# Kernel optimization log

Measured on AMD Instinct MI355X. Metric: run time of the kernel, lower is better.

## Reference

```python
import jax, jax.numpy as jnp
import numpy as np

N = 50000          # nodes
E = 800000         # edges (before self-loops)
G = 64             # graphs in the batch
IN, HID, HEADS, OUT = 512, 128, 2, 64
NEG_SLOPE = 0.2
BN_EPS = 1e-5


def gat_conv(x, src, dst, W, a_src, a_dst, b, concat):
    """PyG-style GATConv (shared lin for src/dst, leaky-relu scoring,
    segment-softmax over incoming edges per destination node)."""
    n = x.shape[0]
    H, C = a_src.shape
    xl = (x @ W).reshape(n, H, C)                      # [N,H,C]
    es = (xl * a_src).sum(-1)                          # [N,H] alpha_src
    ed = (xl * a_dst).sum(-1)                          # [N,H] alpha_dst
    e = jax.nn.leaky_relu(es[src] + ed[dst], NEG_SLOPE)  # [E,H]
    m = jax.ops.segment_max(e, dst, num_segments=n)    # stable softmax
    ex = jnp.exp(e - m[dst])
    den = jax.ops.segment_sum(ex, dst, num_segments=n)
    alpha = ex / (den[dst] + 1e-16)                    # [E,H]
    out = jax.ops.segment_sum(xl[src] * alpha[:, :, None], dst, num_segments=n)
    out = out.reshape(n, H * C) if concat else out.mean(axis=1)
    return out + b


def batch_norm(x, g, b):
    mu = x.mean(axis=0)
    var = x.var(axis=0)  # biased, as torch BN uses for normalization
    return (x - mu) * jax.lax.rsqrt(var + BN_EPS) * g + b


def setup_inputs() -> dict:
    key = jax.random.key(0)
    ks = jax.random.split(key, 24)
    HC = HID * HEADS
    inp = {
        'x': jax.random.normal(ks[0], (N, IN), jnp.float32),
        'edge_index': jax.random.randint(ks[1], (2, E), 0, N, jnp.int64) if jax.config.jax_enable_x64 else jax.random.randint(ks[1], (2, E), 0, N).astype(jnp.int32),
        'batch': jnp.sort(jax.random.randint(ks[2], (N,), 0, G)).astype(jnp.int32),
        # conv1: 512 -> (2,128) concat -> 256
        'W1': jax.random.normal(ks[3], (IN, HC), jnp.float32) * (1.0 / np.sqrt(IN)),
        'as1': jax.random.normal(ks[4], (HEADS, HID), jnp.float32) * 0.05,
        'ad1': jax.random.normal(ks[5], (HEADS, HID), jnp.float32) * 0.05,
        'b1': jnp.zeros((HC,), jnp.float32),
        'g1': jnp.ones((HC,), jnp.float32),
        'be1': jnp.zeros((HC,), jnp.float32),
        # conv2: 256 -> (2,128) concat -> 256
        'W2': jax.random.normal(ks[6], (HC, HC), jnp.float32) * (1.0 / np.sqrt(HC)),
        'as2': jax.random.normal(ks[7], (HEADS, HID), jnp.float32) * 0.05,
        'ad2': jax.random.normal(ks[8], (HEADS, HID), jnp.float32) * 0.05,
        'b2': jnp.zeros((HC,), jnp.float32),
        'g2': jnp.ones((HC,), jnp.float32),
        'be2': jnp.zeros((HC,), jnp.float32),
        # conv3: 256 -> (1,128) mean -> 128
        'W3': jax.random.normal(ks[9], (HC, HID), jnp.float32) * (1.0 / np.sqrt(HC)),
        'as3': jax.random.normal(ks[10], (1, HID), jnp.float32) * 0.05,
        'ad3': jax.random.normal(ks[11], (1, HID), jnp.float32) * 0.05,
        'b3': jnp.zeros((HID,), jnp.float32),
        # final linear 128 -> 64
        'Wlin': jax.random.normal(ks[12], (HID, OUT), jnp.float32) * (1.0 / np.sqrt(HID)),
        'blin': jnp.zeros((OUT,), jnp.float32),
    }
    return inp


def reference(x, edge_index, batch, W1, as1, ad1, b1, g1, be1,
              W2, as2, ad2, b2, g2, be2, W3, as3, ad3, b3, Wlin, blin):
    # add self-loops (PyG GATConv default)
    loop = jnp.arange(N, dtype=edge_index.dtype)
    src = jnp.concatenate([edge_index[0], loop])
    dst = jnp.concatenate([edge_index[1], loop])

    h = gat_conv(x, src, dst, W1, as1, ad1, b1, concat=True)
    h = jax.nn.relu(batch_norm(h, g1, be1))           # dropout: eval mode (identity)
    h = gat_conv(h, src, dst, W2, as2, ad2, b2, concat=True)
    h = jax.nn.relu(batch_norm(h, g2, be2))
    h = gat_conv(h, src, dst, W3, as3, ad3, b3, concat=False)  # [N,128]

    # global mean pool over graphs
    cnt = jax.ops.segment_sum(jnp.ones((N,), h.dtype), batch, num_segments=G)
    pooled = jax.ops.segment_sum(h, batch, num_segments=G) / jnp.maximum(cnt, 1.0)[:, None]
    return pooled @ Wlin + blin                        # [G,64]
```

## Files before the change

### kernel.cpp

```cpp
#include <hip/hip_runtime.h>
#include <cstdint>
#include <math.h>

#define NN 50000
#define EE 800000
#define GG 64
#define NEG_SLOPE 0.2f
#define BN_EPS 1e-5f

typedef short bf16x8 __attribute__((ext_vector_type(8)));
typedef float f32x4 __attribute__((ext_vector_type(4)));

__global__ void k_memset32(int* p, int val, int n) {
    int i = blockIdx.x * blockDim.x + threadIdx.x;
    int stride = gridDim.x * blockDim.x;
    for (; i < n; i += stride) p[i] = val;
}

__device__ inline float leaky(float x) { return x > 0.f ? x : NEG_SLOPE * x; }

__device__ inline unsigned short f2bf(float f) {
    union { float f; uint32_t u; } v;
    v.f = f;
    uint32_t u = v.u;
    return (unsigned short)((u + 0x7fffu + ((u >> 16) & 1u)) >> 16);
}

__device__ inline float bf2f(unsigned short u) {
    union { uint32_t u; float f; } v;
    v.u = (uint32_t)u << 16;
    return v.f;
}
__device__ inline float bflo(uint32_t u) { return __uint_as_float(u << 16); }
__device__ inline float bfhi(uint32_t u) { return __uint_as_float(u & 0xffff0000u); }
__device__ inline uint32_t packbf(float a, float b) {
    return (uint32_t)f2bf(a) | ((uint32_t)f2bf(b) << 16);
}

__device__ inline unsigned char f2fp8(float v) {
    int p = __builtin_amdgcn_cvt_pk_fp8_f32(v, v, 0, false);
    return (unsigned char)(p & 0xff);
}

__device__ inline void gload16(const void* g, void* l) {
    __builtin_amdgcn_global_load_lds(
        (const __attribute__((address_space(1))) unsigned int*)g,
        (__attribute__((address_space(3))) unsigned int*)l, 16, 0, 0);
}

__global__ void k_convert_bf16(const float* __restrict__ in, unsigned short* __restrict__ out,
                               int n4) {
    int i = blockIdx.x * blockDim.x + threadIdx.x;
    int stride = gridDim.x * blockDim.x;
    for (; i < n4; i += stride) {
        float4 v = ((const float4*)in)[i];
        uint2 o;
        o.x = packbf(v.x, v.y);
        o.y = packbf(v.z, v.w);
        ((uint2*)out)[i] = o;
    }
}

__global__ void k_transpose_all(const float* __restrict__ W1, const float* __restrict__ W2,
                                const float* __restrict__ W3, unsigned short* __restrict__ Wt1,
                                unsigned short* __restrict__ Wt2, unsigned short* __restrict__ Wt3) {
    int idx = blockIdx.x * 256 + threadIdx.x;
    if (idx < 512 * 256) {
        int k = idx >> 8, m_ = idx & 255;
        Wt1[(size_t)m_ * 512 + k] = f2bf(W1[idx]);
    } else if (idx < 512 * 256 + 256 * 256) {
        int i = idx - 512 * 256;
        int k = i >> 8, m_ = i & 255;
        Wt2[(size_t)m_ * 256 + k] = f2bf(W2[i]);
    } else if (idx < 512 * 256 + 256 * 256 + 256 * 128) {
        int i = idx - (512 * 256 + 256 * 256);
        int k = i >> 7, m_ = i & 127;
        Wt3[(size_t)m_ * 256 + k] = f2bf(W3[i]);
    }
}

__global__ __launch_bounds__(256) void k_gemm_mfma(
        const unsigned short* __restrict__ A, const unsigned short* __restrict__ Bt,
        unsigned char* __restrict__ C8,
        const float* __restrict__ asrc, const float* __restrict__ adst,
        float* __restrict__ es, float* __restrict__ ed,
        int NR, int K, int M, int H, int gxc) {
    __shared__ unsigned short As[2][128 * 32];
    __shared__ unsigned short Bs[2][128 * 32];
    __shared__ float esA[2][128], edA[2][128];
    int tid = threadIdx.x;
    int wave = tid >> 6, lane = tid & 63;
    int r16 = lane & 15, kg = lane >> 4;
    int wr = wave >> 1, wc = wave & 1;

    int nwg = gridDim.x;
    int nb = blockIdx.x;
    int q = nwg >> 3, r = nwg & 7;
    int xcd = nb & 7, ii = nb >> 3;
    int w = (xcd < r ? xcd * (q + 1) : r * (q + 1) + (xcd - r) * q) + ii;
    int rowBase = (w / gxc) * 128;
    int colBase = (w % gxc) * 128;

    const unsigned short* gA[2];
    const unsigned short* gB[2];
#pragma unroll
    for (int it = 0; it < 2; ++it) {
        int j = it * 256 + tid;
        int row = j >> 2, slot = j & 3;
        int ss = slot ^ ((row >> 1) & 3);
        int rg = rowBase + row;
        if (rg >= NR) rg = NR - 1;
        gA[it] = A + (size_t)rg * K + ss * 8;
        gB[it] = Bt + (size_t)(colBase + row) * K + ss * 8;
    }

    auto STAGE = [&](int buf, int k0) {
#pragma unroll
        for (int it = 0; it < 2; ++it) {
            unsigned short* lbase = &As[buf][(it * 256 + wave * 64) * 8];
            gload16(gA[it] + k0, lbase);
            unsigned short* lbase2 = &Bs[buf][(it * 256 + wave * 64) * 8];
            gload16(gB[it] + k0, lbase2);
        }
    };

    f32x4 acc[4][4] = {};
    int nt = K >> 5;
    STAGE(0, 0);
    __syncthreads();
    for (int t = 0; t < nt; ++t) {
        int cur = t & 1;
        if (t + 1 < nt) STAGE(cur ^ 1, (t + 1) << 5);
        bf16x8 af[4], bfr[4];
#pragma unroll
        for (int m = 0; m < 4; m++) {
            int row = wr * 64 + m * 16 + r16;
            af[m] = *(const bf16x8*)&As[cur][row * 32 + (kg ^ ((row >> 1) & 3)) * 8];
        }
#pragma unroll
        for (int n = 0; n < 4; n++) {
            int row = wc * 64 + n * 16 + r16;
            bfr[n] = *(const bf16x8*)&Bs[cur][row * 32 + (kg ^ ((row >> 1) & 3)) * 8];
        }
#pragma unroll
        for (int m = 0; m < 4; m++)
#pragma unroll
            for (int n = 0; n < 4; n++)
                acc[m][n] = __builtin_amdgcn_mfma_f32_16x16x32_bf16(af[m], bfr[n], acc[m][n], 0, 0, 0);
        __syncthreads();
    }
    int crow0 = rowBase + wr * 64;
    int ccol = colBase + wc * 64 + r16;
#pragma unroll
    for (int m = 0; m < 4; m++) {
#pragma unroll
        for (int j = 0; j < 4; j++) {
            int row = crow0 + m * 16 + kg * 4 + j;
            if (row < NR) {
#pragma unroll
                for (int n = 0; n < 4; n++)
                    C8[(size_t)row * M + ccol + n * 16] = f2fp8(acc[m][n][j]);
            }
        }
    }
    int h_blk = colBase >> 7;
    float as_[4], ad_[4];
#pragma unroll
    for (int n = 0; n < 4; n++) {
        int ch = wc * 64 + n * 16 + r16;
        as_[n] = asrc[h_blk * 128 + ch];
        ad_[n] = adst[h_blk * 128 + ch];
    }
#pragma unroll
    for (int m = 0; m < 4; m++) {
#pragma unroll
        for (int j = 0; j < 4; j++) {
            float e1 = 0.f, e2 = 0.f;
#pragma unroll
            for (int n = 0; n < 4; n++) {
                e1 += acc[m][n][j] * as_[n];
                e2 += acc[m][n][j] * ad_[n];
            }
#pragma unroll
            for (int mask = 1; mask < 16; mask <<= 1) {
                e1 += __shfl_xor(e1, mask, 64);
                e2 += __shfl_xor(e2, mask, 64);
            }
            if (r16 == 0) {
                int lr = wr * 64 + m * 16 + kg * 4 + j;
                esA[wc][lr] = e1;
                edA[wc][lr] = e2;
            }
        }
    }
    __syncthreads();
    if (tid < 128) {
        int row = rowBase + tid;
        if (row < NR) {
            es[row * H + h_blk] = esA[0][tid] + esA[1][tid];
            ed[row * H + h_blk] = edA[0][tid] + edA[1][tid];
        }
    }
}

template <int VEC>
__device__ inline void edge_load(const unsigned char* rp, uint2& w) {
    if constexpr (VEC == 8) {
        w = *(const uint2*)rp;
    } else {
        w.x = *(const unsigned int*)rp;
        w.y = 0;
    }
}

template <int VEC>
__device__ inline void edge_acc(float* acc, float e, const uint2& w) {
    auto p0 = __builtin_amdgcn_cvt_pk_f32_fp8(w.x, false);
    auto p1 = __builtin_amdgcn_cvt_pk_f32_fp8(w.x, true);
    acc[0] += e * p0[0]; acc[1] += e * p0[1];
    acc[2] += e * p1[0]; acc[3] += e * p1[1];
    if constexpr (VEC == 8) {
        auto p2 = __builtin_amdgcn_cvt_pk_f32_fp8(w.y, false);
        auto p3 = __builtin_amdgcn_cvt_pk_f32_fp8(w.y, true);
        acc[4] += e * p2[0]; acc[5] += e * p2[1];
        acc[6] += e * p3[0]; acc[7] += e * p3[1];
    }
}

template <int VEC, int H>
__global__ __launch_bounds__(256) void k_aggregate(
        const unsigned char* __restrict__ xl, const float* __restrict__ es,
        const float* __restrict__ ed, const int* __restrict__ offsets,
        const int* __restrict__ count, const int* __restrict__ ssrc,
        const float* __restrict__ bias, unsigned short* __restrict__ out) {
    const int M = 32 * VEC;
    int wid = threadIdx.x >> 6;
    int n = blockIdx.x * 4 + wid;
    if (n >= NN) return;
    int lane = threadIdx.x & 63;
    int half = lane >> 5, l32 = lane & 31;
    int c0 = l32 * VEC;
    int h = (H == 2) ? (c0 >> 7) : 0;

    float edn0, edn1 = 0.f, self0, self1 = 0.f;
    if constexpr (H == 2) {
        float2 edp = *(const float2*)&ed[n * 2];
        float2 esp = *(const float2*)&es[n * 2];
        edn0 = edp.x; edn1 = edp.y;
        self0 = __expf(leaky(esp.x + edn0));
        self1 = __expf(leaky(esp.y + edn1));
    } else {
        edn0 = ed[n];
        self0 = __expf(leaky(es[n] + edn0));
    }
    float ex_self = (H == 2 && h == 1) ? self1 : self0;

    float acc[VEC] = {};
    if (half == 0) {
        uint2 w;
        edge_load<VEC>(xl + (size_t)n * M + c0, w);
        edge_acc<VEC>(acc, ex_self, w);
    }

    __shared__ int ls[4][64];
    __shared__ float le[4][H][64];
    float den0 = 0.f, den1 = 0.f;
    int s0 = offsets[n], cnt = count[n];
    for (int base = 0; base < cnt; base += 64) {
        int i = base + lane;
        int s = 0;
        float e0 = 0.f, e1 = 0.f;
        if (i < cnt) {
            s = ssrc[s0 + i];
            if constexpr (H == 2) {
                float2 esp = *(const float2*)&es[s * 2];
                e0 = __expf(leaky(esp.x + edn0)); den0 += e0;
                e1 = __expf(leaky(esp.y + edn1)); den1 += e1;
            } else {
                e0 = __expf(leaky(es[s] + edn0)); den0 += e0;
            }
        }
        ls[wid][lane] = s;
        le[wid][0][lane] = e0;
        if constexpr (H == 2) le[wid][1][lane] = e1;
        asm volatile("s_waitcnt lgkmcnt(0)" ::: "memory");
        int lim = min(64, cnt - base);
        int j = half;
        for (; j + 7 < lim; j += 8) {
            int sA = ls[wid][j], sB = ls[wid][j + 2], sC = ls[wid][j + 4], sD = ls[wid][j + 6];
            float eA = le[wid][h][j], eB = le[wid][h][j + 2];
            float eC = le[wid][h][j + 4], eD = le[wid][h][j + 6];
            uint2 wA, wB, wC, wD;
            edge_load<VEC>(xl + (size_t)sA * M + c0, wA);
            edge_load<VEC>(xl + (size_t)sB * M + c0, wB);
            edge_load<VEC>(xl + (size_t)sC * M + c0, wC);
            edge_load<VEC>(xl + (size_t)sD * M + c0, wD);
            edge_acc<VEC>(acc, eA, wA);
            edge_acc<VEC>(acc, eB, wB);
            edge_acc<VEC>(acc, eC, wC);
            edge_acc<VEC>(acc, eD, wD);
        }
        for (; j < lim; j += 2) {
            int sA = ls[wid][j];
            float eA = le[wid][h][j];
            uint2 wA;
            edge_load<VEC>(xl + (size_t)sA * M + c0, wA);
            edge_acc<VEC>(acc, eA, wA);
        }
    }

#pragma unroll
    for (int off = 32; off > 0; off >>= 1) {
        den0 += __shfl_xor(den0, off, 64);
        if constexpr (H == 2) den1 += __shfl_xor(den1, off, 64);
    }
#pragma unroll
    for (int v = 0; v < VEC; v++) acc[v] += __shfl_xor(acc[v], 32, 64);

    float den = ((H == 2 && h == 1) ? den1 : den0) + ex_self + 1e-16f;
    float inv = 1.f / den;
    if (half == 0) {
        unsigned short* op = out + (size_t)n * M + c0;
        if constexpr (VEC == 8) {
            uint4 o;
            o.x = packbf(acc[0] * inv + bias[c0 + 0], acc[1] * inv + bias[c0 + 1]);
            o.y = packbf(acc[2] * inv + bias[c0 + 2], acc[3] * inv + bias[c0 + 3]);
            o.z = packbf(acc[4] * inv + bias[c0 + 4], acc[5] * inv + bias[c0 + 5]);
            o.w = packbf(acc[6] * inv + bias[c0 + 6], acc[7] * inv + bias[c0 + 7]);
            *(uint4*)op = o;
        } else {
            uint2 o;
            o.x = packbf(acc[0] * inv + bias[c0 + 0], acc[1] * inv + bias[c0 + 1]);
            o.y = packbf(acc[2] * inv + bias[c0 + 2], acc[3] * inv + bias[c0 + 3]);
            *(uint2*)op = o;
        }
    }
}

__global__ void k_count(const int* __restrict__ dst, int* __restrict__ count) {
    int e = blockIdx.x * blockDim.x + threadIdx.x;
    if (e < EE) atomicAdd(&count[dst[e]], 1);
}

__global__ void k_scan_local(const int* __restrict__ in, int* __restrict__ out_excl,
                             int* __restrict__ bsums, int n) {
    __shared__ int s[256];
    int tid = threadIdx.x;
    int i = blockIdx.x * 256 + tid;
    int v = (i < n) ? in[i] : 0;
    s[tid] = v;
    __syncthreads();
    for (int off = 1; off < 256; off <<= 1) {
        int t_ = (tid >= off) ? s[tid - off] : 0;
        __syncthreads();
        s[tid] += t_;
        __syncthreads();
    }
    if (i < n) out_excl[i] = s[tid] - v;
    if (tid == 255) bsums[blockIdx.x] = s[255];
}

__global__ void k_scan_sums(int* __restrict__ b, int n) {
    __shared__ int s[256];
    int tid = threadIdx.x;
    int v = (tid < n) ? b[tid] : 0;
    s[tid] = v;
    __syncthreads();
    for (int off = 1; off < 256; off <<= 1) {
        int t_ = (tid >= off) ? s[tid - off] : 0;
        __syncthreads();
        s[tid] += t_;
        __syncthreads();
    }
    if (tid < n) b[tid] = s[tid] - v;
}

__global__ void k_scan_add(int* __restrict__ out_excl, const int* __restrict__ bsums, int n) {
    int i = blockIdx.x * 256 + threadIdx.x;
    if (i < n) out_excl[i] += bsums[blockIdx.x];
}

__global__ void k_scatter(const int* __restrict__ src, const int* __restrict__ dst,
                          const int* __restrict__ offsets, int* __restrict__ cursor,
                          int* __restrict__ ssrc) {
    int e = blockIdx.x * blockDim.x + threadIdx.x;
    if (e >= EE) return;
    int d = dst[e];
    int p = offsets[d] + atomicAdd(&cursor[d], 1);
    ssrc[p] = src[e];
}

__global__ __launch_bounds__(256) void k_bn_stats(const unsigned short* __restrict__ h,
                                                  float* __restrict__ part) {
    int tid = threadIdx.x;
    int bid = blockIdx.x;
    int c0 = (tid & 31) * 8;
    int rg = tid >> 5;
    float s[8] = {}, s2[8] = {};
    for (int r = bid * 8 + rg; r < NN; r += 2048) {
        uint4 v = *(const uint4*)(h + (size_t)r * 256 + c0);
        float f;
        f = bflo(v.x); s[0] += f; s2[0] += f * f;
        f = bfhi(v.x); s[1] += f; s2[1] += f * f;
        f = bflo(v.y); s[2] += f; s2[2] += f * f;
        f = bfhi(v.y); s[3] += f; s2[3] += f * f;
        f = bflo(v.z); s[4] += f; s2[4] += f * f;
        f = bfhi(v.z); s[5] += f; s2[5] += f * f;
        f = bflo(v.w); s[6] += f; s2[6] += f * f;
        f = bfhi(v.w); s[7] += f; s2[7] += f * f;
    }
    __shared__ float sb[8][256];
#pragma unroll
    for (int v = 0; v < 8; v++) sb[rg][c0 + v] = s[v];
    __syncthreads();
    float tot = 0.f;
#pragma unroll
    for (int g = 0; g < 8; g++) tot += sb[g][tid];
    part[bid * 512 + tid] = tot;
    __syncthreads();
#pragma unroll
    for (int v = 0; v < 8; v++) sb[rg][c0 + v] = s2[v];
    __syncthreads();
    tot = 0.f;
#pragma unroll
    for (int g = 0; g < 8; g++) tot += sb[g][tid];
    part[bid * 512 + 256 + tid] = tot;
}

__global__ void k_bn_finalize(const float* __restrict__ part, const float* __restrict__ g,
                              const float* __restrict__ be, float* __restrict__ scale,
                              float* __restrict__ shift) {
    int t = threadIdx.x;
    float s = 0.f, s2 = 0.f;
    for (int b = 0; b < 256; b++) {
        s += part[b * 512 + t];
        s2 += part[b * 512 + 256 + t];
    }
    float mu = s / (float)NN;
    float var = s2 / (float)NN - mu * mu;
    float sc = g[t] * rsqrtf(var + BN_EPS);
    scale[t] = sc;
    shift[t] = be[t] - mu * sc;
}

__global__ void k_bn_apply(unsigned short* __restrict__ h, const float* __restrict__ scale,
                           const float* __restrict__ shift) {
    int i = blockIdx.x * blockDim.x + threadIdx.x;
    int stride = gridDim.x * blockDim.x;
    int total = NN * 256 / 8;
    uint4* h4 = (uint4*)h;
    for (; i < total; i += stride) {
        uint4 v = h4[i];
        int t = (i * 8) & 255;
        float f0 = fmaxf(bflo(v.x) * scale[t + 0] + shift[t + 0], 0.f);
        float f1 = fmaxf(bfhi(v.x) * scale[t + 1] + shift[t + 1], 0.f);
        float f2 = fmaxf(bflo(v.y) * scale[t + 2] + shift[t + 2], 0.f);
        float f3 = fmaxf(bfhi(v.y) * scale[t + 3] + shift[t + 3], 0.f);
        float f4 = fmaxf(bflo(v.z) * scale[t + 4] + shift[t + 4], 0.f);
        float f5 = fmaxf(bfhi(v.z) * scale[t + 5] + shift[t + 5], 0.f);
        float f6 = fmaxf(bflo(v.w) * scale[t + 6] + shift[t + 6], 0.f);
        float f7 = fmaxf(bfhi(v.w) * scale[t + 7] + shift[t + 7], 0.f);
        v.x = packbf(f0, f1);
        v.y = packbf(f2, f3);
        v.z = packbf(f4, f5);
        v.w = packbf(f6, f7);
        h4[i] = v;
    }
}

#define POOL_ROWS 128
__global__ void k_pool(const unsigned short* __restrict__ h3, const int* __restrict__ batch,
                       float* __restrict__ pooled, int* __restrict__ cnt) {
    int t = threadIdx.x;
    int r0 = blockIdx.x * POOL_ROWS;
    if (r0 >= NN) return;
    int rend = min(r0 + POOL_ROWS, NN);
    float acc = 0.f;
    int c_acc = 0;
    int g_cur = batch[r0];
    for (int r = r0; r < rend; r++) {
        int g = batch[r];
        if (g != g_cur) {
            atomicAdd(&pooled[g_cur * 128 + t], acc);
            if (t == 0) atomicAdd(&cnt[g_cur], c_acc);
            acc = 0.f;
            c_acc = 0;
            g_cur = g;
        }
        acc += bf2f(h3[(size_t)r * 128 + t]);
        c_acc++;
    }
    atomicAdd(&pooled[g_cur * 128 + t], acc);
    if (t == 0) atomicAdd(&cnt[g_cur], c_acc);
}

__global__ void k_final(const float* __restrict__ pooled, const int* __restrict__ cnt,
                        const float* __restrict__ Wlin, const float* __restrict__ blin,
                        float* __restrict__ out) {
    int g = blockIdx.x;
    int o = threadIdx.x;
    float c = (float)max(cnt[g], 1);
    float acc = 0.f;
    for (int k = 0; k < 128; k++) acc += pooled[g * 128 + k] * Wlin[k * 64 + o];
    out[g * 64 + o] = acc / c + blin[o];
}

extern "C" void kernel_launch(void* const* d_in, const int* in_sizes, int n_in,
                              void* d_out, int out_size, void* d_ws, size_t ws_size,
                              hipStream_t stream) {
    const float* x = (const float*)d_in[0];
    const int* ei = (const int*)d_in[1];
    const int* batch = (const int*)d_in[2];
    const float* W1 = (const float*)d_in[3];
    const float* as1 = (const float*)d_in[4];
    const float* ad1 = (const float*)d_in[5];
    const float* b1 = (const float*)d_in[6];
    const float* g1 = (const float*)d_in[7];
    const float* be1 = (const float*)d_in[8];
    const float* W2 = (const float*)d_in[9];
    const float* as2 = (const float*)d_in[10];
    const float* ad2 = (const float*)d_in[11];
    const float* b2 = (const float*)d_in[12];
    const float* g2 = (const float*)d_in[13];
    const float* be2 = (const float*)d_in[14];
    const float* W3 = (const float*)d_in[15];
    const float* as3 = (const float*)d_in[16];
    const float* ad3 = (const float*)d_in[17];
    const float* b3 = (const float*)d_in[18];
    const float* Wlin = (const float*)d_in[19];
    const float* blin = (const float*)d_in[20];
    float* out = (float*)d_out;

    const int* src = ei;
    const int* dst = ei + EE;

    char* ws = (char*)d_ws;
    size_t off = 0;
    auto alloc = [&](size_t bytes) -> void* {
        void* p = (void*)(ws + off);
        off = (off + bytes + 255) & ~(size_t)255;
        return p;
    };
    unsigned short* xb = (unsigned short*)alloc((size_t)NN * 512 * 2);
    unsigned char* xl = (unsigned char*)alloc((size_t)NN * 256);
    unsigned short* hbuf = (unsigned short*)alloc((size_t)NN * 256 * 2);
    unsigned short* Wt1 = (unsigned short*)alloc((size_t)256 * 512 * 2);
    unsigned short* Wt2 = (unsigned short*)alloc((size_t)256 * 256 * 2);
    unsigned short* Wt3 = (unsigned short*)alloc((size_t)128 * 256 * 2);
    float* es = (float*)alloc((size_t)NN * 2 * 4);
    float* ed = (float*)alloc((size_t)NN * 2 * 4);
    int* count = (int*)alloc((size_t)NN * 4);
    int* offsets = (int*)alloc((size_t)NN * 4);
    int* cursor = (int*)alloc((size_t)NN * 4);
    int* ssrc = (int*)alloc((size_t)EE * 4);
    int* bsums = (int*)alloc(256 * 4);
    float* bnpart = (float*)alloc((size_t)256 * 512 * 4);
    float* bnscale = (float*)alloc(256 * 4);
    float* bnshift = (float*)alloc(256 * 4);
    float* pooled = (float*)alloc(64 * 128 * 4);
    int* cnt = (int*)alloc(64 * 4);

    const int EB = (EE + 255) / 256;
    const int NB = (NN + 255) / 256;
    const int AGB = (NN + 3) / 4;
    const int NRB = (NN + 127) / 128;

    k_convert_bf16<<<2048, 256, 0, stream>>>(x, xb, NN * 512 / 4);
    k_transpose_all<<<(512 * 256 + 256 * 256 + 256 * 128 + 255) / 256, 256, 0, stream>>>(
        W1, W2, W3, Wt1, Wt2, Wt3);

    k_memset32<<<64, 256, 0, stream>>>(count, 0, NN);
    k_count<<<EB, 256, 0, stream>>>(dst, count);
    k_scan_local<<<NB, 256, 0, stream>>>(count, offsets, bsums, NN);
    k_scan_sums<<<1, 256, 0, stream>>>(bsums, NB);
    k_scan_add<<<NB, 256, 0, stream>>>(offsets, bsums, NN);
    k_memset32<<<64, 256, 0, stream>>>(cursor, 0, NN);
    k_scatter<<<EB, 256, 0, stream>>>(src, dst, offsets, cursor, ssrc);

    auto bn_relu = [&](unsigned short* h, const float* g_, const float* be_) {
        k_bn_stats<<<256, 256, 0, stream>>>(h, bnpart);
        k_bn_finalize<<<1, 256, 0, stream>>>(bnpart, g_, be_, bnscale, bnshift);
        k_bn_apply<<<1024, 256, 0, stream>>>(h, bnscale, bnshift);
    };

    k_gemm_mfma<<<2 * NRB, 256, 0, stream>>>(xb, Wt1, xl, as1, ad1, es, ed, NN, 512, 256, 2, 2);
    k_aggregate<8, 2><<<AGB, 256, 0, stream>>>(xl, es, ed, offsets, count, ssrc, b1, hbuf);
    bn_relu(hbuf, g1, be1);

    k_gemm_mfma<<<2 * NRB, 256, 0, stream>>>(hbuf, Wt2, xl, as2, ad2, es, ed, NN, 256, 256, 2, 2);
    k_aggregate<8, 2><<<AGB, 256, 0, stream>>>(xl, es, ed, offsets, count, ssrc, b2, hbuf);
    bn_relu(hbuf, g2, be2);

    k_gemm_mfma<<<NRB, 256, 0, stream>>>(hbuf, Wt3, xl, as3, ad3, es, ed, NN, 256, 128, 1, 1);
    k_aggregate<4, 1><<<AGB, 256, 0, stream>>>(xl, es, ed, offsets, count, ssrc, b3, hbuf);

    k_memset32<<<33, 256, 0, stream>>>((int*)pooled, 0, 64 * 128 + 64);
    k_pool<<<(NN + POOL_ROWS - 1) / POOL_ROWS, 128, 0, stream>>>(hbuf, batch, pooled, cnt);
    k_final<<<GG, 64, 0, stream>>>(pooled, cnt, Wlin, blin, out);
}
```

Measured before the change: 430.7 us.

## Fuse mean-pool into final aggregation, merge prep kernels, single-block scan

```diff
diff --git a/kernel.cpp b/kernel.cpp
--- a/kernel.cpp
+++ b/kernel.cpp
@@ -48,34 +48,34 @@
         (__attribute__((address_space(3))) unsigned int*)l, 16, 0, 0);
 }
 
-__global__ void k_convert_bf16(const float* __restrict__ in, unsigned short* __restrict__ out,
-                               int n4) {
-    int i = blockIdx.x * blockDim.x + threadIdx.x;
+__global__ void k_prep(const float* __restrict__ x, unsigned short* __restrict__ xb,
+                       const float* __restrict__ W1, const float* __restrict__ W2,
+                       const float* __restrict__ W3, unsigned short* __restrict__ Wt1,
+                       unsigned short* __restrict__ Wt2, unsigned short* __restrict__ Wt3) {
+    int t0 = blockIdx.x * blockDim.x + threadIdx.x;
     int stride = gridDim.x * blockDim.x;
-    for (; i < n4; i += stride) {
-        float4 v = ((const float4*)in)[i];
+    const int n4 = NN * 512 / 4;
+    for (int i = t0; i < n4; i += stride) {
+        float4 v = ((const float4*)x)[i];
         uint2 o;
         o.x = packbf(v.x, v.y);
         o.y = packbf(v.z, v.w);
-        ((uint2*)out)[i] = o;
-    }
-}
-
-__global__ void k_transpose_all(const float* __restrict__ W1, const float* __restrict__ W2,
-                                const float* __restrict__ W3, unsigned short* __restrict__ Wt1,
-                                unsigned short* __restrict__ Wt2, unsigned short* __restrict__ Wt3) {
-    int idx = blockIdx.x * 256 + threadIdx.x;
-    if (idx < 512 * 256) {
-        int k = idx >> 8, m_ = idx & 255;
-        Wt1[(size_t)m_ * 512 + k] = f2bf(W1[idx]);
-    } else if (idx < 512 * 256 + 256 * 256) {
-        int i = idx - 512 * 256;
-        int k = i >> 8, m_ = i & 255;
-        Wt2[(size_t)m_ * 256 + k] = f2bf(W2[i]);
-    } else if (idx < 512 * 256 + 256 * 256 + 256 * 128) {
-        int i = idx - (512 * 256 + 256 * 256);
-        int k = i >> 7, m_ = i & 127;
-        Wt3[(size_t)m_ * 256 + k] = f2bf(W3[i]);
+        ((uint2*)xb)[i] = o;
+    }
+    const int TR = 512 * 256 + 256 * 256 + 256 * 128;
+    for (int idx = t0; idx < TR; idx += stride) {
+        if (idx < 512 * 256) {
+            int k = idx >> 8, m_ = idx & 255;
+            Wt1[(size_t)m_ * 512 + k] = f2bf(W1[idx]);
+        } else if (idx < 512 * 256 + 256 * 256) {
+            int i = idx - 512 * 256;
+            int k = i >> 8, m_ = i & 255;
+            Wt2[(size_t)m_ * 256 + k] = f2bf(W2[i]);
+        } else {
+            int i = idx - (512 * 256 + 256 * 256);
+            int k = i >> 7, m_ = i & 127;
+            Wt3[(size_t)m_ * 256 + k] = f2bf(W3[i]);
+        }
     }
 }
 
@@ -227,12 +227,13 @@
     }
 }
 
-template <int VEC, int H>
+template <int VEC, int H, bool POOL>
 __global__ __launch_bounds__(256) void k_aggregate(
         const unsigned char* __restrict__ xl, const float* __restrict__ es,
         const float* __restrict__ ed, const int* __restrict__ offsets,
         const int* __restrict__ count, const int* __restrict__ ssrc,
-        const float* __restrict__ bias, unsigned short* __restrict__ out) {
+        const float* __restrict__ bias, unsigned short* __restrict__ out,
+        const int* __restrict__ batch, float* __restrict__ pooled, int* __restrict__ cnt) {
     const int M = 32 * VEC;
     int wid = threadIdx.x >> 6;
     int n = blockIdx.x * 4 + wid;
@@ -265,12 +266,12 @@
     __shared__ int ls[4][64];
     __shared__ float le[4][H][64];
     float den0 = 0.f, den1 = 0.f;
-    int s0 = offsets[n], cnt = count[n];
-    for (int base = 0; base < cnt; base += 64) {
+    int s0 = offsets[n], cnte = count[n];
+    for (int base = 0; base < cnte; base += 64) {
         int i = base + lane;
         int s = 0;
         float e0 = 0.f, e1 = 0.f;
-        if (i < cnt) {
+        if (i < cnte) {
             s = ssrc[s0 + i];
             if constexpr (H == 2) {
                 float2 esp = *(const float2*)&es[s * 2];
@@ -284,7 +285,7 @@
         le[wid][0][lane] = e0;
         if constexpr (H == 2) le[wid][1][lane] = e1;
         asm volatile("s_waitcnt lgkmcnt(0)" ::: "memory");
-        int lim = min(64, cnt - base);
+        int lim = min(64, cnte - base);
         int j = half;
         for (; j + 7 < lim; j += 8) {
             int sA = ls[wid][j], sB = ls[wid][j + 2], sC = ls[wid][j + 4], sD = ls[wid][j + 6];
@@ -320,19 +321,27 @@
     float den = ((H == 2 && h == 1) ? den1 : den0) + ex_self + 1e-16f;
     float inv = 1.f / den;
     if (half == 0) {
-        unsigned short* op = out + (size_t)n * M + c0;
-        if constexpr (VEC == 8) {
-            uint4 o;
-            o.x = packbf(acc[0] * inv + bias[c0 + 0], acc[1] * inv + bias[c0 + 1]);
-            o.y = packbf(acc[2] * inv + bias[c0 + 2], acc[3] * inv + bias[c0 + 3]);
-            o.z = packbf(acc[4] * inv + bias[c0 + 4], acc[5] * inv + bias[c0 + 5]);
-            o.w = packbf(acc[6] * inv + bias[c0 + 6], acc[7] * inv + bias[c0 + 7]);
-            *(uint4*)op = o;
+        if constexpr (POOL) {
+            int g = batch[n];
+            if (lane == 0) atomicAdd(&cnt[g], 1);
+#pragma unroll
+            for (int v = 0; v < VEC; v++)
+                atomicAdd(&pooled[g * 128 + c0 + v], acc[v] * inv + bias[c0 + v]);
         } else {
-            uint2 o;
-            o.x = packbf(acc[0] * inv + bias[c0 + 0], acc[1] * inv + bias[c0 + 1]);
-            o.y = packbf(acc[2] * inv + bias[c0 + 2], acc[3] * inv + bias[c0 + 3]);
-            *(uint2*)op = o;
+            unsigned short* op = out + (size_t)n * M + c0;
+            if constexpr (VEC == 8) {
+                uint4 o;
+                o.x = packbf(acc[0] * inv + bias[c0 + 0], acc[1] * inv + bias[c0 + 1]);
+                o.y = packbf(acc[2] * inv + bias[c0 + 2], acc[3] * inv + bias[c0 + 3]);
+                o.z = packbf(acc[4] * inv + bias[c0 + 4], acc[5] * inv + bias[c0 + 5]);
+                o.w = packbf(acc[6] * inv + bias[c0 + 6], acc[7] * inv + bias[c0 + 7]);
+                *(uint4*)op = o;
+            } else {
+                uint2 o;
+                o.x = packbf(acc[0] * inv + bias[c0 + 0], acc[1] * inv + bias[c0 + 1]);
+                o.y = packbf(acc[2] * inv + bias[c0 + 2], acc[3] * inv + bias[c0 + 3]);
+                *(uint2*)op = o;
+            }
         }
     }
 }
@@ -342,42 +351,38 @@
     if (e < EE) atomicAdd(&count[dst[e]], 1);
 }
 
-__global__ void k_scan_local(const int* __restrict__ in, int* __restrict__ out_excl,
-                             int* __restrict__ bsums, int n) {
-    __shared__ int s[256];
+__global__ __launch_bounds__(1024) void k_scan(const int* __restrict__ in,
+                                               int* __restrict__ out, int n) {
+    __shared__ int wsum[16];
     int tid = threadIdx.x;
-    int i = blockIdx.x * 256 + tid;
-    int v = (i < n) ? in[i] : 0;
-    s[tid] = v;
-    __syncthreads();
-    for (int off = 1; off < 256; off <<= 1) {
-        int t_ = (tid >= off) ? s[tid - off] : 0;
+    int wid = tid >> 6, lane = tid & 63;
+    int carry = 0;
+    for (int base = 0; base < n; base += 1024) {
+        int i = base + tid;
+        int v = (i < n) ? in[i] : 0;
+        int x = v;
+#pragma unroll
+        for (int off = 1; off < 64; off <<= 1) {
+            int y = __shfl_up(x, off, 64);
+            if (lane >= off) x += y;
+        }
+        if (lane == 63) wsum[wid] = x;
         __syncthreads();
-        s[tid] += t_;
+        if (wid == 0) {
+            int t = (lane < 16) ? wsum[lane] : 0;
+#pragma unroll
+            for (int off = 1; off < 16; off <<= 1) {
+                int y = __shfl_up(t, off, 64);
+                if (lane >= off) t += y;
+            }
+            if (lane < 16) wsum[lane] = t;
+        }
         __syncthreads();
-    }
-    if (i < n) out_excl[i] = s[tid] - v;
-    if (tid == 255) bsums[blockIdx.x] = s[255];
-}
-
-__global__ void k_scan_sums(int* __restrict__ b, int n) {
-    __shared__ int s[256];
-    int tid = threadIdx.x;
-    int v = (tid < n) ? b[tid] : 0;
-    s[tid] = v;
-    __syncthreads();
-    for (int off = 1; off < 256; off <<= 1) {
-        int t_ = (tid >= off) ? s[tid - off] : 0;
+        int woff = (wid > 0) ? wsum[wid - 1] : 0;
+        if (i < n) out[i] = carry + woff + x - v;
+        carry += wsum[15];
         __syncthreads();
-        s[tid] += t_;
-        __syncthreads();
-    }
-    if (tid < n) b[tid] = s[tid] - v;
-}
-
-__global__ void k_scan_add(int* __restrict__ out_excl, const int* __restrict__ bsums, int n) {
-    int i = blockIdx.x * 256 + threadIdx.x;
-    if (i < n) out_excl[i] += bsums[blockIdx.x];
+    }
 }
 
 __global__ void k_scatter(const int* __restrict__ src, const int* __restrict__ dst,
@@ -466,32 +471,6 @@
         v.w = packbf(f6, f7);
         h4[i] = v;
     }
-}
-
-#define POOL_ROWS 128
-__global__ void k_pool(const unsigned short* __restrict__ h3, const int* __restrict__ batch,
-                       float* __restrict__ pooled, int* __restrict__ cnt) {
-    int t = threadIdx.x;
-    int r0 = blockIdx.x * POOL_ROWS;
-    if (r0 >= NN) return;
-    int rend = min(r0 + POOL_ROWS, NN);
-    float acc = 0.f;
-    int c_acc = 0;
-    int g_cur = batch[r0];
-    for (int r = r0; r < rend; r++) {
-        int g = batch[r];
-        if (g != g_cur) {
-            atomicAdd(&pooled[g_cur * 128 + t], acc);
-            if (t == 0) atomicAdd(&cnt[g_cur], c_acc);
-            acc = 0.f;
-            c_acc = 0;
-            g_cur = g;
-        }
-        acc += bf2f(h3[(size_t)r * 128 + t]);
-        c_acc++;
-    }
-    atomicAdd(&pooled[g_cur * 128 + t], acc);
-    if (t == 0) atomicAdd(&cnt[g_cur], c_acc);
 }
 
 __global__ void k_final(const float* __restrict__ pooled, const int* __restrict__ cnt,
@@ -549,11 +528,11 @@
     unsigned short* Wt3 = (unsigned short*)alloc((size_t)128 * 256 * 2);
     float* es = (float*)alloc((size_t)NN * 2 * 4);
     float* ed = (float*)alloc((size_t)NN * 2 * 4);
-    int* count = (int*)alloc((size_t)NN * 4);
+    int* cc = (int*)alloc((size_t)2 * NN * 4);
+    int* count = cc;
+    int* cursor = cc + NN;
     int* offsets = (int*)alloc((size_t)NN * 4);
-    int* cursor = (int*)alloc((size_t)NN * 4);
     int* ssrc = (int*)alloc((size_t)EE * 4);
-    int* bsums = (int*)alloc(256 * 4);
     float* bnpart = (float*)alloc((size_t)256 * 512 * 4);
     float* bnscale = (float*)alloc(256 * 4);
     float* bnshift = (float*)alloc(256 * 4);
@@ -561,20 +540,14 @@
     int* cnt = (int*)alloc(64 * 4);
 
     const int EB = (EE + 255) / 256;
-    const int NB = (NN + 255) / 256;
     const int AGB = (NN + 3) / 4;
     const int NRB = (NN + 127) / 128;
 
-    k_convert_bf16<<<2048, 256, 0, stream>>>(x, xb, NN * 512 / 4);
-    k_transpose_all<<<(512 * 256 + 256 * 256 + 256 * 128 + 255) / 256, 256, 0, stream>>>(
-        W1, W2, W3, Wt1, Wt2, Wt3);
-
-    k_memset32<<<64, 256, 0, stream>>>(count, 0, NN);
+    k_prep<<<2048, 256, 0, stream>>>(x, xb, W1, W2, W3, Wt1, Wt2, Wt3);
+
+    k_memset32<<<128, 256, 0, stream>>>(cc, 0, 2 * NN);
     k_count<<<EB, 256, 0, stream>>>(dst, count);
-    k_scan_local<<<NB, 256, 0, stream>>>(count, offsets, bsums, NN);
-    k_scan_sums<<<1, 256, 0, stream>>>(bsums, NB);
-    k_scan_add<<<NB, 256, 0, stream>>>(offsets, bsums, NN);
-    k_memset32<<<64, 256, 0, stream>>>(cursor, 0, NN);
+    k_scan<<<1, 1024, 0, stream>>>(count, offsets, NN);
     k_scatter<<<EB, 256, 0, stream>>>(src, dst, offsets, cursor, ssrc);
 
     auto bn_relu = [&](unsigned short* h, const float* g_, const float* be_) {
@@ -584,17 +557,19 @@
     };
 
     k_gemm_mfma<<<2 * NRB, 256, 0, stream>>>(xb, Wt1, xl, as1, ad1, es, ed, NN, 512, 256, 2, 2);
-    k_aggregate<8, 2><<<AGB, 256, 0, stream>>>(xl, es, ed, offsets, count, ssrc, b1, hbuf);
+    k_aggregate<8, 2, false><<<AGB, 256, 0, stream>>>(xl, es, ed, offsets, count, ssrc, b1,
+                                                      hbuf, nullptr, nullptr, nullptr);
     bn_relu(hbuf, g1, be1);
 
     k_gemm_mfma<<<2 * NRB, 256, 0, stream>>>(hbuf, Wt2, xl, as2, ad2, es, ed, NN, 256, 256, 2, 2);
-    k_aggregate<8, 2><<<AGB, 256, 0, stream>>>(xl, es, ed, offsets, count, ssrc, b2, hbuf);
+    k_aggregate<8, 2, false><<<AGB, 256, 0, stream>>>(xl, es, ed, offsets, count, ssrc, b2,
+                                                      hbuf, nullptr, nullptr, nullptr);
     bn_relu(hbuf, g2, be2);
 
+    k_memset32<<<33, 256, 0, stream>>>((int*)pooled, 0, 64 * 128 + 64);
     k_gemm_mfma<<<NRB, 256, 0, stream>>>(hbuf, Wt3, xl, as3, ad3, es, ed, NN, 256, 128, 1, 1);
-    k_aggregate<4, 1><<<AGB, 256, 0, stream>>>(xl, es, ed, offsets, count, ssrc, b3, hbuf);
-
-    k_memset32<<<33, 256, 0, stream>>>((int*)pooled, 0, 64 * 128 + 64);
-    k_pool<<<(NN + POOL_ROWS - 1) / POOL_ROWS, 128, 0, stream>>>(hbuf, batch, pooled, cnt);
+    k_aggregate<4, 1, true><<<AGB, 256, 0, stream>>>(xl, es, ed, offsets, count, ssrc, b3,
+                                                     nullptr, batch, pooled, cnt);
+
     k_final<<<GG, 64, 0, stream>>>(pooled, cnt, Wlin, blin, out);
 }
```

Result: slower. 760.0 us (+76.5%).
